# Kernel tuning notes

Measured on AMD Instinct MI355X. Metric: run time of the kernel, lower is better.

The kernel has to match this reference:

```python
import math
import jax, jax.numpy as jnp
import numpy as np

STRIDE = 8
IMG = 2048
NA = 9            # num anchors per cell (len(cfg['anchor_size']))
NC = 80           # num classes
TOPK = 1000
CONF = 0.05
NMS_T = 0.6
CTR_CLAMP = 32.0
EXP_CLAMP = math.log(1e8)            # DEFAULT_EXP_CLAMP
SCALE_CLAMP = math.log(1000.0 / 16)  # DEFAULT_SCALE_CLAMP


def setup_inputs() -> dict:
    key = jax.random.key(0)
    k1, k2, k3 = jax.random.split(key, 3)
    H = W = IMG // STRIDE  # 256
    obj_pred = jax.random.normal(k1, (1, NA, H, W), jnp.float32)
    cls_pred = jax.random.normal(k2, (1, NA * NC, H, W), jnp.float32)
    reg_pred = jax.random.normal(k3, (1, NA * 4, H, W), jnp.float32) * 0.5
    # generate_anchors: grid centers (+0.5)*stride, tiled anchor sizes -> [H*W*NA, 4] (cx,cy,w,h)
    ys, xs = jnp.meshgrid(jnp.arange(H), jnp.arange(W), indexing='ij')
    xy = (jnp.stack([xs, ys], -1).reshape(-1, 2).astype(jnp.float32) + 0.5) * STRIDE
    sizes = jnp.array([[32, 32], [64, 64], [128, 128], [32, 64], [64, 128],
                       [128, 256], [64, 32], [128, 64], [256, 128]], jnp.float32)
    anchor_boxes = jnp.concatenate(
        [jnp.repeat(xy[:, None, :], NA, axis=1),
         jnp.broadcast_to(sizes[None], (H * W, NA, 2))], axis=-1).reshape(-1, 4)
    return {"obj_pred": obj_pred, "cls_pred": cls_pred,
            "reg_pred": reg_pred, "anchor_boxes": anchor_boxes}


def _detect(obj_pred, cls_pred, reg_pred, anchor_boxes):
    B, _, H, W = obj_pred.shape
    obj = obj_pred.reshape(B, NA, 1, H, W)
    cls = cls_pred.reshape(B, NA, NC, H, W)
    # normalized_cls_pred = cls + obj - log(1 + exp(clamp(cls)) + exp(clamp(obj)))
    norm = cls + obj - jnp.log(1.0 + jnp.exp(jnp.minimum(cls, EXP_CLAMP))
                               + jnp.exp(jnp.minimum(obj, EXP_CLAMP)))
    norm = norm.transpose(0, 3, 4, 1, 2).reshape(B, -1, NC)[0]          # [M, NC]
    reg = reg_pred.reshape(B, NA, 4, H, W).transpose(0, 3, 4, 1, 2).reshape(B, -1, 4)[0]  # [M, 4]
    prob = jax.nn.sigmoid(norm)
    scores_all = prob.max(axis=-1)
    labels_all = prob.argmax(axis=-1)
    scores, idx = jax.lax.top_k(scores_all, TOPK)                        # descending
    labels = labels_all[idx]
    reg = reg[idx]
    anc = anchor_boxes[idx]
    # decode_boxes
    ctr_off = jnp.clip(reg[..., :2] * anc[..., 2:], -CTR_CLAMP, CTR_CLAMP)
    ctr = anc[..., :2] + ctr_off
    wh = anc[..., 2:] * jnp.exp(jnp.minimum(reg[..., 2:], SCALE_CLAMP))
    boxes = jnp.concatenate([ctr - 0.5 * wh, ctr + 0.5 * wh], axis=-1)
    boxes = jnp.clip(boxes / IMG, 0.0, 1.0)
    return scores, labels, boxes


def _nms_keep(scores, labels, boxes):
    # scores are sorted descending; per-class greedy NMS == class-masked global greedy NMS
    valid = scores >= CONF
    x1, y1, x2, y2 = boxes[:, 0], boxes[:, 1], boxes[:, 2], boxes[:, 3]
    areas = (x2 - x1) * (y2 - y1)
    xx1 = jnp.maximum(x1[:, None], x1[None, :])
    yy1 = jnp.maximum(y1[:, None], y1[None, :])
    xx2 = jnp.minimum(x2[:, None], x2[None, :])
    yy2 = jnp.minimum(y2[:, None], y2[None, :])
    inter = jnp.maximum(1e-28, xx2 - xx1) * jnp.maximum(1e-28, yy2 - yy1)
    iou = inter / (areas[:, None] + areas[None, :] - inter + 1e-14)      # [N, N]
    sup = (iou > NMS_T) & (labels[:, None] == labels[None, :])
    later = jnp.arange(TOPK)[None, :] > jnp.arange(TOPK)[:, None]

    def body(i, keep):
        row = sup[i] & later[i] & keep[i]   # i suppresses only if still kept
        return keep & ~row

    return jax.lax.fori_loop(0, TOPK, body, valid)


def reference(obj_pred, cls_pred, reg_pred, anchor_boxes):
    scores, labels, boxes = _detect(obj_pred, cls_pred, reg_pred, anchor_boxes)
    keep = _nms_keep(scores, labels, boxes)
    # fixed-shape outputs: detections sorted by score with a keep mask
    return scores, labels, boxes, keep
```

## Files before the change

kernel.cpp:

```cpp
#include <hip/hip_runtime.h>
#include <stdint.h>

#define NA 9
#define NC 80
#define NTOT 589824
#define TOPK 1000
#define CONF 0.05f
#define NMS_T 0.6
#define CTR_CLAMP 32.0
#define IMGF 2048.0
#define SCALE_CLAMP 4.135166556742356

#define KEYS_OFF   0u
#define LABELS_OFF 4718592u
#define HIST_OFF   7077888u
#define CNT_OFF    7143424u
#define CUTB_OFF   7143428u
#define CAND_OFF   7143680u
#define TOPIDX_OFF 7176448u
#define BOXES_OFF  7180448u
#define LABS_OFF   7196448u
#define SUP_OFF    7200448u
#define SUPB_OFF   7331520u

__device__ __forceinline__ float cexpf(float x) {
#pragma clang fp contract(off)
  float m = floorf(__builtin_fmaf(x, 1.44269504088896341f, 0.5f));
  float r = __builtin_fmaf(m, -0.693359375f, x);
  r = __builtin_fmaf(m, 2.12194440e-4f, r);
  float r2 = r * r;
  float y = 1.9875691500E-4f;
  y = __builtin_fmaf(y, r, 1.3981999507E-3f);
  y = __builtin_fmaf(y, r, 8.3334519073E-3f);
  y = __builtin_fmaf(y, r, 4.1665795894E-2f);
  y = __builtin_fmaf(y, r, 1.6666665459E-1f);
  y = __builtin_fmaf(y, r, 5.0000001201E-1f);
  y = __builtin_fmaf(y, r2, r) + 1.0f;
  return ldexpf(y, (int)m);
}

__device__ __forceinline__ float clogf_(float xin) {
#pragma clang fp contract(off)
  unsigned b = __float_as_uint(xin);
  int e = (int)(b >> 23) - 126;
  float m = __uint_as_float((b & 0x007FFFFFu) | 0x3F000000u);
  if (m < 0.707106781186547524f) { e -= 1; m = m + m; }
  float x = m - 1.0f;
  float z = x * x;
  float y = 7.0376836292E-2f;
  y = __builtin_fmaf(y, x, -1.1514610310E-1f);
  y = __builtin_fmaf(y, x, 1.1676998740E-1f);
  y = __builtin_fmaf(y, x, -1.2420140846E-1f);
  y = __builtin_fmaf(y, x, 1.4249322787E-1f);
  y = __builtin_fmaf(y, x, -1.6668057665E-1f);
  y = __builtin_fmaf(y, x, 2.0000714765E-1f);
  y = __builtin_fmaf(y, x, -2.4999993993E-1f);
  y = __builtin_fmaf(y, x, 3.3333331174E-1f);
  y = y * x * z;
  float ef = (float)e;
  y = __builtin_fmaf(ef, -2.12194440e-4f, y);
  y = __builtin_fmaf(-0.5f, z, y);
  float res = x + y;
  res = __builtin_fmaf(ef, 0.693359375f, res);
  return res;
}

__global__ __launch_bounds__(256) void k_score(const float4* __restrict__ obj4,
                                               const float4* __restrict__ cls4,
                                               unsigned long long* __restrict__ keys_all,
                                               int* __restrict__ labels_all) {
#pragma clang fp contract(off)
  int t = blockIdx.x * 256 + threadIdx.x;
  int a = t >> 14;
  int rem = t & 16383;
  float4 ov = obj4[t];
  float ob[4] = {ov.x, ov.y, ov.z, ov.w};
  float best[4] = {-1e30f, -1e30f, -1e30f, -1e30f};
  int bc[4] = {0, 0, 0, 0};
  const float4* cp = cls4 + a * 80 * 16384 + rem;
#pragma unroll 8
  for (int c = 0; c < 80; c++) {
    float4 cv = cp[c * 16384];
    float cl[4] = {cv.x, cv.y, cv.z, cv.w};
#pragma unroll
    for (int k = 0; k < 4; k++) {
      if (cl[k] > best[k]) { best[k] = cl[k]; bc[k] = c; }
    }
  }
  unsigned long long kv[4];
  int lv[4];
#pragma unroll
  for (int k = 0; k < 4; k++) {
    float c = best[k], o = ob[k];
    float ec = cexpf(c);
    float eo = cexpf(o);
    float L = clogf_((1.0f + ec) + eo);
    float nrm = (c + o) - L;
    float p = 1.0f / (1.0f + cexpf(-nrm));
    unsigned j = (unsigned)((rem * 4 + k) * 9 + a);
    unsigned bits = __float_as_uint(p);
    kv[k] = ((unsigned long long)bits << 20) | (unsigned long long)(0xFFFFFu - j);
    lv[k] = bc[k];
  }
  unsigned po = (unsigned)(a * 65536 + rem * 4);
#pragma unroll
  for (int k = 0; k < 4; k++) { keys_all[po + k] = kv[k]; labels_all[po + k] = lv[k]; }
}

__global__ __launch_bounds__(256) void k_hist(const unsigned* __restrict__ keys_hi,
                                              unsigned* __restrict__ hist) {
  __shared__ unsigned lh[16384];
  int tid = threadIdx.x;
  for (int b = tid; b < 16384; b += 256) lh[b] = 0u;
  __syncthreads();
  for (int t = blockIdx.x * 256 + tid; t < NTOT; t += 512 * 256) {
    unsigned hi = keys_hi[2 * t + 1];
    atomicAdd(&lh[hi >> 4], 1u);
  }
  __syncthreads();
  for (int b = tid; b < 16384; b += 256) {
    unsigned v = lh[b];
    if (v) atomicAdd(&hist[b], v);
  }
}

__global__ __launch_bounds__(1024) void k_cutoff(const unsigned* __restrict__ hist,
                                                 unsigned* __restrict__ cutB) {
  __shared__ unsigned suf[1024];
  __shared__ int sC;
  __shared__ unsigned sAbove;
  int tid = threadIdx.x;
  unsigned s = 0;
  for (int b = 0; b < 16; b++) s += hist[tid * 16 + b];
  unsigned v = s;
  suf[tid] = v;
  __syncthreads();
  for (int off = 1; off < 1024; off <<= 1) {
    unsigned add = (tid + off < 1024) ? suf[tid + off] : 0u;
    __syncthreads();
    v += add;
    suf[tid] = v;
    __syncthreads();
  }
  unsigned nxt = (tid < 1023) ? suf[tid + 1] : 0u;
  if (v >= TOPK && nxt < TOPK) { sC = tid; sAbove = nxt; }
  __syncthreads();
  int C = sC;
  unsigned above = sAbove;
  if (tid < 16) {
    unsigned acc = above;
    for (int b = 15; b >= tid; b--) acc += hist[C * 16 + b];
    unsigned h = hist[C * 16 + tid];
    if (acc >= TOPK && (tid == 15 || (acc - h) < TOPK)) *cutB = (unsigned)(C * 16 + tid);
  }
}

__global__ __launch_bounds__(256) void k_compact(const unsigned long long* __restrict__ keys_all,
                                                 const unsigned* __restrict__ cutB,
                                                 unsigned* __restrict__ cand_cnt,
                                                 unsigned long long* __restrict__ cand) {
  unsigned t = blockIdx.x * 256 + threadIdx.x;
  unsigned long long key = keys_all[t];
  bool win = (unsigned)(key >> 36) >= *cutB;
  unsigned long long m = __ballot(win);
  if (m == 0ull) return;
  int lane = threadIdx.x & 63;
  int leader = __ffsll((long long)m) - 1;
  unsigned base = 0;
  if (lane == leader) base = atomicAdd(cand_cnt, (unsigned)__popcll(m));
  base = __shfl(base, leader, 64);
  if (win) {
    unsigned pos = base + (unsigned)__popcll(m & ((1ull << lane) - 1ull));
    if (pos < 4096u) cand[pos] = key;
  }
}

__global__ __launch_bounds__(1024) void k_sort(const unsigned* __restrict__ cand_cnt,
                                               const unsigned long long* __restrict__ cand,
                                               float* __restrict__ out_scores,
                                               unsigned* __restrict__ topidx) {
  __shared__ unsigned long long key[4096];
  int tid = threadIdx.x;
  unsigned M = *cand_cnt;
  if (M > 4096u) M = 4096u;
  for (int p = 0; p < 4; p++) {
    int t = p * 1024 + tid;
    key[t] = (t < (int)M) ? cand[t] : 0ull;
  }
  __syncthreads();
  for (int k = 2; k <= 4096; k <<= 1) {
    for (int j = k >> 1; j > 0; j >>= 1) {
      for (int p = 0; p < 4; p++) {
        int t = p * 1024 + tid;
        int px = t ^ j;
        if (px > t) {
          unsigned long long x = key[t], y = key[px];
          bool desc = ((t & k) == 0);
          if (desc ? (x < y) : (x > y)) { key[t] = y; key[px] = x; }
        }
      }
      __syncthreads();
    }
  }
  for (int r = tid; r < TOPK; r += 1024) {
    unsigned long long kk = key[r];
    out_scores[r] = __uint_as_float((unsigned)(kk >> 20));
    topidx[r] = 0xFFFFFu - (unsigned)(kk & 0xFFFFFull);
  }
}

__global__ __launch_bounds__(256) void k_decode(const unsigned* __restrict__ topidx,
                                                const int* __restrict__ labels_all,
                                                const float* __restrict__ reg_pred,
                                                const float* __restrict__ anchors,
                                                float* __restrict__ out,
                                                float* __restrict__ boxes_s,
                                                int* __restrict__ labels_s) {
  int r = blockIdx.x * 256 + threadIdx.x;
  if (r >= TOPK) return;
  unsigned idx = topidx[r];
  unsigned hw = idx / 9u;
  unsigned a = idx - hw * 9u;
  int lab = labels_all[a * 65536u + hw];
  unsigned base = a * 4u * 65536u + hw;
  double r0 = (double)reg_pred[base];
  double r1 = (double)reg_pred[base + 65536u];
  double r2 = (double)reg_pred[base + 131072u];
  double r3 = (double)reg_pred[base + 196608u];
  double ax = (double)anchors[idx * 4u + 0], ay = (double)anchors[idx * 4u + 1];
  double aw = (double)anchors[idx * 4u + 2], ah = (double)anchors[idx * 4u + 3];
  double ox = fmin(fmax(r0 * aw, -CTR_CLAMP), CTR_CLAMP);
  double oy = fmin(fmax(r1 * ah, -CTR_CLAMP), CTR_CLAMP);
  double cx = ax + ox, cy = ay + oy;
  double ww = aw * exp(fmin(r2, SCALE_CLAMP));
  double hh = ah * exp(fmin(r3, SCALE_CLAMP));
  float x1 = (float)fmin(fmax((cx - 0.5 * ww) * (1.0 / IMGF), 0.0), 1.0);
  float y1 = (float)fmin(fmax((cy - 0.5 * hh) * (1.0 / IMGF), 0.0), 1.0);
  float x2 = (float)fmin(fmax((cx + 0.5 * ww) * (1.0 / IMGF), 0.0), 1.0);
  float y2 = (float)fmin(fmax((cy + 0.5 * hh) * (1.0 / IMGF), 0.0), 1.0);
  out[1000 + r] = (float)lab;
  out[2000 + 4 * r + 0] = x1;
  out[2000 + 4 * r + 1] = y1;
  out[2000 + 4 * r + 2] = x2;
  out[2000 + 4 * r + 3] = y2;
  boxes_s[4 * r + 0] = x1;
  boxes_s[4 * r + 1] = y1;
  boxes_s[4 * r + 2] = x2;
  boxes_s[4 * r + 3] = y2;
  labels_s[r] = lab;
}

__global__ __launch_bounds__(256) void k_sup(const float* __restrict__ boxes_s,
                                             const int* __restrict__ labels_s,
                                             unsigned long long* __restrict__ sup,
                                             unsigned long long* __restrict__ supB) {
  __shared__ float bx[4000];
  __shared__ int lb[1000];
  int i = blockIdx.x;
  int tid = threadIdx.x;
  for (int t = tid; t < 4000; t += 256) bx[t] = boxes_s[t];
  for (int t = tid; t < 1000; t += 256) lb[t] = labels_s[t];
  __syncthreads();
  double ix1 = (double)bx[4 * i], iy1 = (double)bx[4 * i + 1];
  double ix2 = (double)bx[4 * i + 2], iy2 = (double)bx[4 * i + 3];
  double ia = (ix2 - ix1) * (iy2 - iy1);
  int il = lb[i];
  for (int rep = 0; rep < 4; rep++) {
    int j = rep * 256 + tid;
    bool s = false;
    if (j < TOPK && j > i && lb[j] == il) {
      double jx1 = (double)bx[4 * j], jy1 = (double)bx[4 * j + 1];
      double jx2 = (double)bx[4 * j + 2], jy2 = (double)bx[4 * j + 3];
      double xx1 = fmax(ix1, jx1), yy1 = fmax(iy1, jy1);
      double xx2 = fmin(ix2, jx2), yy2 = fmin(iy2, jy2);
      double inter = fmax(1e-28, xx2 - xx1) * fmax(1e-28, yy2 - yy1);
      double ja = (jx2 - jx1) * (jy2 - jy1);
      double iou = inter / (ia + ja - inter + 1e-14);
      s = iou > NMS_T;
    }
    unsigned long long w = __ballot(s);
    if ((tid & 63) == 0) {
      int wi = rep * 4 + (tid >> 6);
      sup[i * 16 + wi] = w;
      supB[wi * 1024 + i] = w;
    }
  }
}

__device__ __forceinline__ unsigned long long shflxor64(unsigned long long v, int m) {
  unsigned lo = __shfl_xor((unsigned)v, m, 64);
  unsigned hi = __shfl_xor((unsigned)(v >> 32), m, 64);
  return ((unsigned long long)hi << 32) | lo;
}

__global__ __launch_bounds__(64) void k_nms(const unsigned long long* __restrict__ supB,
                                            const float* __restrict__ scores,
                                            float* __restrict__ keep_out) {
  int lane = threadIdx.x;
  unsigned long long inval[16];
#pragma unroll
  for (int m = 0; m < 16; m++) {
    int j = m * 64 + lane;
    bool bad = (j >= TOPK) || (scores[j] < CONF);
    inval[m] = __ballot(bad);
  }
  unsigned long long kept[16];
#pragma unroll
  for (int b = 0; b < 16; b++) {
    unsigned long long acc = 0ull;
#pragma unroll
    for (int m = 0; m < b; m++) {
      unsigned long long r = supB[b * 1024 + m * 64 + lane];
      if ((kept[m] >> lane) & 1ull) acc |= r;
    }
    if (b > 0) {
#pragma unroll
      for (int s = 1; s < 64; s <<= 1) acc |= shflxor64(acc, s);
    }
    unsigned alo = __builtin_amdgcn_readfirstlane((unsigned)acc);
    unsigned ahi = __builtin_amdgcn_readfirstlane((unsigned)(acc >> 32));
    unsigned long long cur = inval[b] | (((unsigned long long)ahi << 32) | alo);
    unsigned long long diag = supB[b * 1024 + b * 64 + lane];
    unsigned dlo = (unsigned)diag, dhi = (unsigned)(diag >> 32);
#pragma unroll 8
    for (int k = 0; k < 64; k++) {
      unsigned rlo = __builtin_amdgcn_readlane(dlo, k);
      unsigned rhi = __builtin_amdgcn_readlane(dhi, k);
      unsigned long long rk = ((unsigned long long)rhi << 32) | rlo;
      unsigned long long take = ((cur >> k) & 1ull) ? 0ull : rk;
      cur |= take;
    }
    kept[b] = ~cur;
  }
#pragma unroll
  for (int m = 0; m < 16; m++) {
    int j = m * 64 + lane;
    if (j < TOPK) keep_out[j] = ((kept[m] >> lane) & 1ull) ? 1.0f : 0.0f;
  }
}

extern "C" void kernel_launch(void* const* d_in, const int* in_sizes, int n_in,
                              void* d_out, int out_size, void* d_ws, size_t ws_size,
                              hipStream_t stream) {
  const float* obj = (const float*)d_in[0];
  const float* cls = (const float*)d_in[1];
  const float* reg = (const float*)d_in[2];
  const float* anc = (const float*)d_in[3];
  float* out = (float*)d_out;
  char* ws = (char*)d_ws;

  unsigned long long* keys_all = (unsigned long long*)(ws + KEYS_OFF);
  int* labels_all = (int*)(ws + LABELS_OFF);
  unsigned* hist = (unsigned*)(ws + HIST_OFF);
  unsigned* cand_cnt = (unsigned*)(ws + CNT_OFF);
  unsigned* cutB = (unsigned*)(ws + CUTB_OFF);
  unsigned long long* cand = (unsigned long long*)(ws + CAND_OFF);
  unsigned* topidx = (unsigned*)(ws + TOPIDX_OFF);
  float* boxes_s = (float*)(ws + BOXES_OFF);
  int* labels_s = (int*)(ws + LABS_OFF);
  unsigned long long* sup = (unsigned long long*)(ws + SUP_OFF);
  unsigned long long* supB = (unsigned long long*)(ws + SUPB_OFF);

  hipMemsetAsync(ws + HIST_OFF, 0, 65536 + 512, stream);

  k_score<<<576, 256, 0, stream>>>((const float4*)obj, (const float4*)cls, keys_all, labels_all);
  k_hist<<<512, 256, 0, stream>>>((const unsigned*)keys_all, hist);
  k_cutoff<<<1, 1024, 0, stream>>>(hist, cutB);
  k_compact<<<2304, 256, 0, stream>>>(keys_all, cutB, cand_cnt, cand);
  k_sort<<<1, 1024, 0, stream>>>(cand_cnt, cand, out, topidx);
  k_decode<<<4, 256, 0, stream>>>(topidx, labels_all, reg, anc, out, boxes_s, labels_s);
  k_sup<<<1000, 256, 0, stream>>>(boxes_s, labels_s, sup, supB);
  k_nms<<<1, 64, 0, stream>>>(supB, out, out + 6000);
}
```

Measured before the change: 434.2 us.

## Fuse histogram into scoring, replace bitonic sort with rank-and-decode kernel

Builds the score histogram inside the scoring kernel through shared-memory atomics, which removes the separate histogram pass. The kernel now stores 32-bit score bits instead of 64-bit keys, and the key is built only for candidates during compaction. The single-block bitonic sort and the decode kernel are replaced by a 16-block rank-by-counting kernel that decodes boxes directly at each candidate's rank. The redundant row-major suppression matrix write is also dropped. In exchange, each scoring block zeroes and flushes a 64KB shared histogram, which may lower occupancy.

Result: no change. 431.2 us (-0.7%).

```diff
diff --git a/kernel.cpp b/kernel.cpp
--- a/kernel.cpp
+++ b/kernel.cpp
@@ -11,17 +11,15 @@
 #define IMGF 2048.0
 #define SCALE_CLAMP 4.135166556742356
 
-#define KEYS_OFF   0u
-#define LABELS_OFF 4718592u
-#define HIST_OFF   7077888u
-#define CNT_OFF    7143424u
-#define CUTB_OFF   7143428u
-#define CAND_OFF   7143680u
-#define TOPIDX_OFF 7176448u
-#define BOXES_OFF  7180448u
-#define LABS_OFF   7196448u
-#define SUP_OFF    7200448u
-#define SUPB_OFF   7331520u
+#define BITS_OFF   0u
+#define LABELS_OFF 2359296u
+#define HIST_OFF   4718592u
+#define CNT_OFF    4784128u
+#define CUTB_OFF   4784132u
+#define CAND_OFF   4784384u
+#define BOXES_OFF  4817152u
+#define LABS_OFF   4833152u
+#define SUPB_OFF   4837376u
 
 __device__ __forceinline__ float cexpf(float x) {
 #pragma clang fp contract(off)
@@ -67,10 +65,15 @@
 
 __global__ __launch_bounds__(256) void k_score(const float4* __restrict__ obj4,
                                                const float4* __restrict__ cls4,
-                                               unsigned long long* __restrict__ keys_all,
-                                               int* __restrict__ labels_all) {
+                                               unsigned* __restrict__ bits_all,
+                                               int* __restrict__ labels_all,
+                                               unsigned* __restrict__ hist) {
 #pragma clang fp contract(off)
-  int t = blockIdx.x * 256 + threadIdx.x;
+  __shared__ unsigned lh[16384];
+  int tid = threadIdx.x;
+  for (int b = tid; b < 16384; b += 256) lh[b] = 0u;
+  __syncthreads();
+  int t = blockIdx.x * 256 + tid;
   int a = t >> 14;
   int rem = t & 16383;
   float4 ov = obj4[t];
@@ -87,8 +90,7 @@
       if (cl[k] > best[k]) { best[k] = cl[k]; bc[k] = c; }
     }
   }
-  unsigned long long kv[4];
-  int lv[4];
+  unsigned bv[4];
 #pragma unroll
   for (int k = 0; k < 4; k++) {
     float c = best[k], o = ob[k];
@@ -97,26 +99,12 @@
     float L = clogf_((1.0f + ec) + eo);
     float nrm = (c + o) - L;
     float p = 1.0f / (1.0f + cexpf(-nrm));
-    unsigned j = (unsigned)((rem * 4 + k) * 9 + a);
-    unsigned bits = __float_as_uint(p);
-    kv[k] = ((unsigned long long)bits << 20) | (unsigned long long)(0xFFFFFu - j);
-    lv[k] = bc[k];
+    bv[k] = __float_as_uint(p);
+    atomicAdd(&lh[bv[k] >> 16], 1u);
   }
   unsigned po = (unsigned)(a * 65536 + rem * 4);
 #pragma unroll
-  for (int k = 0; k < 4; k++) { keys_all[po + k] = kv[k]; labels_all[po + k] = lv[k]; }
-}
-
-__global__ __launch_bounds__(256) void k_hist(const unsigned* __restrict__ keys_hi,
-                                              unsigned* __restrict__ hist) {
-  __shared__ unsigned lh[16384];
-  int tid = threadIdx.x;
-  for (int b = tid; b < 16384; b += 256) lh[b] = 0u;
-  __syncthreads();
-  for (int t = blockIdx.x * 256 + tid; t < NTOT; t += 512 * 256) {
-    unsigned hi = keys_hi[2 * t + 1];
-    atomicAdd(&lh[hi >> 4], 1u);
-  }
+  for (int k = 0; k < 4; k++) { bits_all[po + k] = bv[k]; labels_all[po + k] = bc[k]; }
   __syncthreads();
   for (int b = tid; b < 16384; b += 256) {
     unsigned v = lh[b];
@@ -155,13 +143,13 @@
   }
 }
 
-__global__ __launch_bounds__(256) void k_compact(const unsigned long long* __restrict__ keys_all,
+__global__ __launch_bounds__(256) void k_compact(const unsigned* __restrict__ bits_all,
                                                  const unsigned* __restrict__ cutB,
                                                  unsigned* __restrict__ cand_cnt,
                                                  unsigned long long* __restrict__ cand) {
   unsigned t = blockIdx.x * 256 + threadIdx.x;
-  unsigned long long key = keys_all[t];
-  bool win = (unsigned)(key >> 36) >= *cutB;
+  unsigned bits = bits_all[t];
+  bool win = (bits >> 16) >= *cutB;
   unsigned long long m = __ballot(win);
   if (m == 0ull) return;
   int lane = threadIdx.x & 63;
@@ -170,89 +158,76 @@
   if (lane == leader) base = atomicAdd(cand_cnt, (unsigned)__popcll(m));
   base = __shfl(base, leader, 64);
   if (win) {
+    unsigned a = t >> 16;
+    unsigned hw = t & 65535u;
+    unsigned j = hw * 9u + a;
     unsigned pos = base + (unsigned)__popcll(m & ((1ull << lane) - 1ull));
-    if (pos < 4096u) cand[pos] = key;
-  }
-}
-
-__global__ __launch_bounds__(1024) void k_sort(const unsigned* __restrict__ cand_cnt,
-                                               const unsigned long long* __restrict__ cand,
-                                               float* __restrict__ out_scores,
-                                               unsigned* __restrict__ topidx) {
-  __shared__ unsigned long long key[4096];
+    if (pos < 4096u)
+      cand[pos] = ((unsigned long long)bits << 20) | (unsigned long long)(0xFFFFFu - j);
+  }
+}
+
+__global__ __launch_bounds__(256) void k_rank(const unsigned* __restrict__ cand_cnt,
+                                              const unsigned long long* __restrict__ cand,
+                                              const int* __restrict__ labels_all,
+                                              const float* __restrict__ reg_pred,
+                                              const float* __restrict__ anchors,
+                                              float* __restrict__ out,
+                                              float* __restrict__ boxes_s,
+                                              int* __restrict__ labels_s) {
+  __shared__ unsigned long long lkey[256];
   int tid = threadIdx.x;
+  int c = blockIdx.x * 256 + tid;
   unsigned M = *cand_cnt;
   if (M > 4096u) M = 4096u;
-  for (int p = 0; p < 4; p++) {
-    int t = p * 1024 + tid;
-    key[t] = (t < (int)M) ? cand[t] : 0ull;
-  }
-  __syncthreads();
-  for (int k = 2; k <= 4096; k <<= 1) {
-    for (int j = k >> 1; j > 0; j >>= 1) {
-      for (int p = 0; p < 4; p++) {
-        int t = p * 1024 + tid;
-        int px = t ^ j;
-        if (px > t) {
-          unsigned long long x = key[t], y = key[px];
-          bool desc = ((t & k) == 0);
-          if (desc ? (x < y) : (x > y)) { key[t] = y; key[px] = x; }
-        }
-      }
-      __syncthreads();
-    }
-  }
-  for (int r = tid; r < TOPK; r += 1024) {
-    unsigned long long kk = key[r];
-    out_scores[r] = __uint_as_float((unsigned)(kk >> 20));
-    topidx[r] = 0xFFFFFu - (unsigned)(kk & 0xFFFFFull);
-  }
-}
-
-__global__ __launch_bounds__(256) void k_decode(const unsigned* __restrict__ topidx,
-                                                const int* __restrict__ labels_all,
-                                                const float* __restrict__ reg_pred,
-                                                const float* __restrict__ anchors,
-                                                float* __restrict__ out,
-                                                float* __restrict__ boxes_s,
-                                                int* __restrict__ labels_s) {
-  int r = blockIdx.x * 256 + threadIdx.x;
-  if (r >= TOPK) return;
-  unsigned idx = topidx[r];
-  unsigned hw = idx / 9u;
-  unsigned a = idx - hw * 9u;
-  int lab = labels_all[a * 65536u + hw];
-  unsigned base = a * 4u * 65536u + hw;
-  double r0 = (double)reg_pred[base];
-  double r1 = (double)reg_pred[base + 65536u];
-  double r2 = (double)reg_pred[base + 131072u];
-  double r3 = (double)reg_pred[base + 196608u];
-  double ax = (double)anchors[idx * 4u + 0], ay = (double)anchors[idx * 4u + 1];
-  double aw = (double)anchors[idx * 4u + 2], ah = (double)anchors[idx * 4u + 3];
-  double ox = fmin(fmax(r0 * aw, -CTR_CLAMP), CTR_CLAMP);
-  double oy = fmin(fmax(r1 * ah, -CTR_CLAMP), CTR_CLAMP);
-  double cx = ax + ox, cy = ay + oy;
-  double ww = aw * exp(fmin(r2, SCALE_CLAMP));
-  double hh = ah * exp(fmin(r3, SCALE_CLAMP));
-  float x1 = (float)fmin(fmax((cx - 0.5 * ww) * (1.0 / IMGF), 0.0), 1.0);
-  float y1 = (float)fmin(fmax((cy - 0.5 * hh) * (1.0 / IMGF), 0.0), 1.0);
-  float x2 = (float)fmin(fmax((cx + 0.5 * ww) * (1.0 / IMGF), 0.0), 1.0);
-  float y2 = (float)fmin(fmax((cy + 0.5 * hh) * (1.0 / IMGF), 0.0), 1.0);
-  out[1000 + r] = (float)lab;
-  out[2000 + 4 * r + 0] = x1;
-  out[2000 + 4 * r + 1] = y1;
-  out[2000 + 4 * r + 2] = x2;
-  out[2000 + 4 * r + 3] = y2;
-  boxes_s[4 * r + 0] = x1;
-  boxes_s[4 * r + 1] = y1;
-  boxes_s[4 * r + 2] = x2;
-  boxes_s[4 * r + 3] = y2;
-  labels_s[r] = lab;
+  unsigned long long mykey = (c < (int)M) ? cand[c] : 0ull;
+  unsigned rank = 0;
+  for (int tile = 0; tile < 16; tile++) {
+    __syncthreads();
+    int src = tile * 256 + tid;
+    lkey[tid] = (src < (int)M) ? cand[src] : 0ull;
+    __syncthreads();
+#pragma unroll 8
+    for (int q = 0; q < 256; q++) rank += (lkey[q] > mykey) ? 1u : 0u;
+  }
+  if (c < (int)M && rank < TOPK) {
+    int r = (int)rank;
+    unsigned j = 0xFFFFFu - (unsigned)(mykey & 0xFFFFFull);
+    unsigned hw = j / 9u;
+    unsigned a = j - hw * 9u;
+    int lab = labels_all[a * 65536u + hw];
+    unsigned base = a * 4u * 65536u + hw;
+    double r0 = (double)reg_pred[base];
+    double r1 = (double)reg_pred[base + 65536u];
+    double r2 = (double)reg_pred[base + 131072u];
+    double r3 = (double)reg_pred[base + 196608u];
+    double ax = (double)anchors[j * 4u + 0], ay = (double)anchors[j * 4u + 1];
+    double aw = (double)anchors[j * 4u + 2], ah = (double)anchors[j * 4u + 3];
+    double ox = fmin(fmax(r0 * aw, -CTR_CLAMP), CTR_CLAMP);
+    double oy = fmin(fmax(r1 * ah, -CTR_CLAMP), CTR_CLAMP);
+    double cx = ax + ox, cy = ay + oy;
+    double ww = aw * exp(fmin(r2, SCALE_CLAMP));
+    double hh = ah * exp(fmin(r3, SCALE_CLAMP));
+    float x1 = (float)fmin(fmax((cx - 0.5 * ww) * (1.0 / IMGF), 0.0), 1.0);
+    float y1 = (float)fmin(fmax((cy - 0.5 * hh) * (1.0 / IMGF), 0.0), 1.0);
+    float x2 = (float)fmin(fmax((cx + 0.5 * ww) * (1.0 / IMGF), 0.0), 1.0);
+    float y2 = (float)fmin(fmax((cy + 0.5 * hh) * (1.0 / IMGF), 0.0), 1.0);
+    out[r] = __uint_as_float((unsigned)(mykey >> 20));
+    out[1000 + r] = (float)lab;
+    out[2000 + 4 * r + 0] = x1;
+    out[2000 + 4 * r + 1] = y1;
+    out[2000 + 4 * r + 2] = x2;
+    out[2000 + 4 * r + 3] = y2;
+    boxes_s[4 * r + 0] = x1;
+    boxes_s[4 * r + 1] = y1;
+    boxes_s[4 * r + 2] = x2;
+    boxes_s[4 * r + 3] = y2;
+    labels_s[r] = lab;
+  }
 }
 
 __global__ __launch_bounds__(256) void k_sup(const float* __restrict__ boxes_s,
                                              const int* __restrict__ labels_s,
-                                             unsigned long long* __restrict__ sup,
                                              unsigned long long* __restrict__ supB) {
   __shared__ float bx[4000];
   __shared__ int lb[1000];
@@ -279,11 +254,7 @@
       s = iou > NMS_T;
     }
     unsigned long long w = __ballot(s);
-    if ((tid & 63) == 0) {
-      int wi = rep * 4 + (tid >> 6);
-      sup[i * 16 + wi] = w;
-      supB[wi * 1024 + i] = w;
-    }
+    if ((tid & 63) == 0) supB[(rep * 4 + (tid >> 6)) * 1024 + i] = w;
   }
 }
 
@@ -349,26 +320,22 @@
   float* out = (float*)d_out;
   char* ws = (char*)d_ws;
 
-  unsigned long long* keys_all = (unsigned long long*)(ws + KEYS_OFF);
+  unsigned* bits_all = (unsigned*)(ws + BITS_OFF);
   int* labels_all = (int*)(ws + LABELS_OFF);
   unsigned* hist = (unsigned*)(ws + HIST_OFF);
   unsigned* cand_cnt = (unsigned*)(ws + CNT_OFF);
   unsigned* cutB = (unsigned*)(ws + CUTB_OFF);
   unsigned long long* cand = (unsigned long long*)(ws + CAND_OFF);
-  unsigned* topidx = (unsigned*)(ws + TOPIDX_OFF);
   float* boxes_s = (float*)(ws + BOXES_OFF);
   int* labels_s = (int*)(ws + LABS_OFF);
-  unsigned long long* sup = (unsigned long long*)(ws + SUP_OFF);
   unsigned long long* supB = (unsigned long long*)(ws + SUPB_OFF);
 
   hipMemsetAsync(ws + HIST_OFF, 0, 65536 + 512, stream);
 
-  k_score<<<576, 256, 0, stream>>>((const float4*)obj, (const float4*)cls, keys_all, labels_all);
-  k_hist<<<512, 256, 0, stream>>>((const unsigned*)keys_all, hist);
+  k_score<<<576, 256, 0, stream>>>((const float4*)obj, (const float4*)cls, bits_all, labels_all, hist);
   k_cutoff<<<1, 1024, 0, stream>>>(hist, cutB);
-  k_compact<<<2304, 256, 0, stream>>>(keys_all, cutB, cand_cnt, cand);
-  k_sort<<<1, 1024, 0, stream>>>(cand_cnt, cand, out, topidx);
-  k_decode<<<4, 256, 0, stream>>>(topidx, labels_all, reg, anc, out, boxes_s, labels_s);
-  k_sup<<<1000, 256, 0, stream>>>(boxes_s, labels_s, sup, supB);
+  k_compact<<<2304, 256, 0, stream>>>(bits_all, cutB, cand_cnt, cand);
+  k_rank<<<16, 256, 0, stream>>>(cand_cnt, cand, labels_all, reg, anc, out, boxes_s, labels_s);
+  k_sup<<<1000, 256, 0, stream>>>(boxes_s, labels_s, supB);
   k_nms<<<1, 64, 0, stream>>>(supB, out, out + 6000);
 }
```
